# Optimization experiments

Measured on AMD Instinct MI355X. Metric: run time of the kernel, lower is better.

## Reference

```python
import jax, jax.numpy as jnp
import numpy as np

B, N_OBJ, K, D_MSG = 1024, 128, 32, 64
Y0 = 0.28209479177387814  # 1/(2*sqrt(pi)), l=0 integral-normalized SH
Y1 = 0.4886025119029199   # sqrt(3/(4*pi)),  l=1 integral-normalized SH


def _sh_lmax1(vec):
    """Spherical harmonics up to l=1, normalize=True, 'integral' normalization. [...,3] -> [...,4]."""
    r = jnp.linalg.norm(vec, axis=-1, keepdims=True)
    u = vec / jnp.maximum(r, 1e-12)
    return jnp.concatenate([jnp.full_like(r, Y0), Y1 * u], axis=-1)


def _forward(inputs, W_msg, W_out):
    Bsz, n, _ = inputs.shape
    masses = inputs[..., 0:1]           # [B,n,1]
    loc = inputs[..., 1:4]              # [B,n,3]
    vel = inputs[..., 4:7]              # [B,n,3]
    # canonicalize_mode == 'com': weights = masses
    w = masses
    com = jnp.sum(w / jnp.sum(w, axis=-2, keepdims=True) * loc, axis=-2, keepdims=True)
    loc = loc - com
    # --- knn_graph per batch element (loop=False, k nearest excluding self) ---
    d2 = jnp.sum((loc[:, :, None, :] - loc[:, None, :, :]) ** 2, axis=-1)  # [B,n,n]
    d2 = jnp.where(jnp.eye(n, dtype=bool)[None], jnp.inf, d2)
    _, nbr = jax.lax.top_k(-d2, K)                                          # [B,n,K]
    offs = (jnp.arange(Bsz) * n)[:, None, None]
    src = (nbr + offs).reshape(-1)                                          # edge_index[0]: neighbor j
    dst = (jnp.broadcast_to(jnp.arange(n)[None, :, None], (Bsz, n, K)) + offs).reshape(-1)  # edge_index[1]: center i
    # --- flatten node tensors ---
    pos = loc.reshape(-1, 3)
    v = vel.reshape(-1, 3)
    m = masses.reshape(-1, 1)
    Nn = Bsz * n
    # --- gravity graph augmentation ---
    rel = pos[src] - pos[dst]
    edge_dist = jnp.linalg.norm(rel, axis=-1, keepdims=True)
    prod_mass = m[src] * m[dst]
    edge_attr = _sh_lmax1(rel)                                              # [E,4]
    vel_emb = _sh_lmax1(v)                                                  # [Nn,4]
    deg = jnp.maximum(jax.ops.segment_sum(jnp.ones(src.shape[0], jnp.float32), dst, num_segments=Nn), 1.0)[:, None]
    node_attr = jax.ops.segment_sum(edge_attr, dst, num_segments=Nn) / deg + vel_emb
    vel_abs = jnp.linalg.norm(v, axis=-1, keepdims=True)
    x = jnp.concatenate([pos, v, vel_abs], axis=-1)                         # [Nn,7]
    amf = jnp.concatenate([edge_dist, prod_mass], axis=-1)                  # [E,2]
    # --- surrogate SEGNN: one message-passing layer ---
    m_in = jnp.concatenate([x[src], x[dst], edge_attr, amf], axis=-1)       # [E,20]
    msg = jax.nn.relu(m_in @ W_msg)                                         # [E,64]
    agg = jax.ops.segment_sum(msg, dst, num_segments=Nn) / deg              # [Nn,64]
    pred_shift = jnp.concatenate([x, node_attr, agg], axis=-1) @ W_out      # [Nn,3]
    return loc + pred_shift.reshape(Bsz, n, 3) + com


def setup_inputs() -> dict:
    key = jax.random.key(0)
    k1, k2, k3 = jax.random.split(key, 3)
    inputs = jax.random.uniform(k1, (B, N_OBJ, 7), dtype=jnp.float32)  # positive masses in col 0
    W_msg = jax.random.normal(k2, (20, D_MSG), dtype=jnp.float32) * 0.1
    W_out = jax.random.normal(k3, (D_MSG + 7 + 4, 3), dtype=jnp.float32) * 0.1
    return {"inputs": inputs, "W_msg": W_msg, "W_out": W_out}


def reference(inputs, W_msg, W_out):
    pred = _forward(inputs, W_msg, W_out)
    return (pred, jnp.zeros(inputs.shape[0], dtype=jnp.float32))
```

## Files before the change

kernel.cpp:

```cpp
#include <hip/hip_runtime.h>

#define NB 1024
#define NN 128
#define KK 32
#define DM 64

constexpr float Y0 = 0.28209479177387814f;
constexpr float Y1 = 0.4886025119029199f;

typedef float f2 __attribute__((ext_vector_type(2)));


__global__ __launch_bounds__(256) void k12_prep_knn(const float* __restrict__ in,
        float* __restrict__ feats, float* __restrict__ com, int* __restrict__ nbr,
        float* __restrict__ out)
{
    const int b = blockIdx.x, t = threadIdx.x;
    const int lane = t & 63, w = t >> 6;
    __shared__ float4 sP[128];
    __shared__ float red[2][4];

    float m=0.f,lx=0.f,ly=0.f,lz=0.f,vx=0.f,vy=0.f,vz=0.f;
    if (t < 128) {
        const float* p = in + ((size_t)b*NN + t)*7;
        m=p[0]; lx=p[1]; ly=p[2]; lz=p[3]; vx=p[4]; vy=p[5]; vz=p[6];
    }
    {
        float sw=m, sx=m*lx, sy=m*ly, sz=m*lz;
        #pragma unroll
        for (int s=1;s<64;s<<=1) {
            sw+=__shfl_xor(sw,s); sx+=__shfl_xor(sx,s);
            sy+=__shfl_xor(sy,s); sz+=__shfl_xor(sz,s);
        }
        if (t<128 && lane==0) { red[w][0]=sw; red[w][1]=sx; red[w][2]=sy; red[w][3]=sz; }
    }
    if (t==0) out[(size_t)NB*NN*3 + b] = 0.f;
    __syncthreads();
    const float Wt  = red[0][0]+red[1][0];
    const float cmx = (red[0][1]+red[1][1])/Wt;
    const float cmy = (red[0][2]+red[1][2])/Wt;
    const float cmz = (red[0][3]+red[1][3])/Wt;
    if (t < 128) {
        const float px=lx-cmx, py=ly-cmy, pz=lz-cmz;
        const float va = sqrtf(vx*vx+vy*vy+vz*vz);
        sP[t] = make_float4(px,py,pz,m);
        float4* f4 = (float4*)(feats + ((size_t)b*NN + t)*8);
        f4[0] = make_float4(px,py,pz,vx);
        f4[1] = make_float4(vy,vz,va,m);
        if (t==0) { float4* c4=(float4*)(com + (size_t)b*4); *c4 = make_float4(cmx,cmy,cmz,0.f); }
    }
    __syncthreads();

    const float4 A4 = sP[lane];
    const float4 B4 = sP[lane+64];
    const float INF = __int_as_float(0x7f800000);
    const unsigned long long lt = (1ULL<<lane)-1ULL;
    #pragma unroll 1
    for (int i=0; i<32; i+=4) {
        const int nb0 = w*32 + i;
        unsigned ua[4], ub[4], P[4];
        #pragma unroll
        for (int k=0;k<4;k++) {
            const int n = nb0 + k;
            const float4 C = sP[n];
            float dx=A4.x-C.x, dy=A4.y-C.y, dz=A4.z-C.z;
            float d2a = dx*dx+dy*dy+dz*dz;
            dx=B4.x-C.x; dy=B4.y-C.y; dz=B4.z-C.z;
            float d2b = dx*dx+dy*dy+dz*dz;
            if (lane    == n) d2a = INF;
            if (lane+64 == n) d2b = INF;
            ua[k]=__float_as_uint(d2a); ub[k]=__float_as_uint(d2b);
            P[k]=0u;
        }
        #pragma unroll 1
        for (int bit=30;bit>=0;--bit) {
            const unsigned msk = 1u<<bit;
            #pragma unroll
            for (int k=0;k<4;k++) {
                const unsigned Q = P[k]|msk;
                const int cnt = __popcll(__ballot(ua[k]<Q)) + __popcll(__ballot(ub[k]<Q));
                if (cnt<=31) P[k]=Q;
            }
        }
        #pragma unroll
        for (int k=0;k<4;k++) {
            const unsigned T = P[k];
            const unsigned long long m0=__ballot(ua[k]<T), m1=__ballot(ub[k]<T);
            const unsigned long long e0=__ballot(ua[k]==T), e1=__ballot(ub[k]==T);
            const int c0n=__popcll(m0), c=c0n+__popcll(m1), rem=32-c;
            int* row = nbr + ((size_t)b*NN + nb0 + k)*32;
            if (ua[k]< T) row[__popcll(m0&lt)] = lane;
            if (ub[k]< T) row[c0n+__popcll(m1&lt)] = lane+64;
            if (ua[k]==T) { const int r=__popcll(e0&lt);               if (r<rem) row[c+r]=lane; }
            if (ub[k]==T) { const int r=__popcll(e0)+__popcll(e1&lt);  if (r<rem) row[c+r]=lane+64; }
        }
    }
}

__global__ __launch_bounds__(256) void k3_main(const float* __restrict__ feats,
        const int* __restrict__ nbr, const float* __restrict__ Wm,
        const float* __restrict__ Wo, const float* __restrict__ com,
        float* __restrict__ out)
{
    const int b = blockIdx.x, t = threadIdx.x;
    __shared__ float4 sPos[128];
    __shared__ float4 sVel[128];
    __shared__ __align__(16) float sXs[128*64];
    __shared__ float  sWm[20][64];
    __shared__ float  sWo[75][3];
    __shared__ float4 sE4[32][33];
    __shared__ float  sPm[32][33];
    __shared__ int    sSrc[32][33];
    __shared__ float4 sSu[32];

    for (int i=t;i<1280;i+=256) ((float*)sWm)[i] = Wm[i];
    for (int i=t;i<225; i+=256) ((float*)sWo)[i] = Wo[i];
    if (t < 128) {
        const float4* f4 = (const float4*)(feats + ((size_t)b*NN + t)*8);
        sPos[t] = f4[0];
        sVel[t] = f4[1];
    }
    __syncthreads();
    if (t < 128) {
        const float4 a = sPos[t], c = sVel[t];
        sPos[t] = make_float4(a.x,a.y,a.z,c.w);
        sVel[t] = make_float4(a.w,c.x,c.y,c.z);
    }
    __syncthreads();

    for (int i=t;i<8192;i+=256) {
        const int n = i>>6, d = i&63;
        const float4 P = sPos[n], V = sVel[n];
        float s = P.x*sWm[0][d];
        s = fmaf(P.y, sWm[1][d], s);
        s = fmaf(P.z, sWm[2][d], s);
        s = fmaf(V.x, sWm[3][d], s);
        s = fmaf(V.y, sWm[4][d], s);
        s = fmaf(V.z, sWm[5][d], s);
        s = fmaf(V.w, sWm[6][d], s);
        const int q = d>>2;
        sXs[(n<<6) + ((q ^ (n&7))<<2) + (d&3)] = s;
    }
    __syncthreads();

    const int dsub = t & 7, ng = t >> 3, d0 = dsub*8, q0 = dsub*2;
    f2 wc2[5][4];
    #pragma unroll
    for (int r=0;r<5;r++)
        #pragma unroll
        for (int j=0;j<4;j++) {
            wc2[r][j].x = sWm[15+r][d0+2*j];
            wc2[r][j].y = sWm[15+r][d0+2*j+1];
        }
    const float cmx = com[(size_t)b*4+0], cmy = com[(size_t)b*4+1], cmz = com[(size_t)b*4+2];

    #pragma unroll 1
    for (int ch=0; ch<4; ++ch) {
        {
            const int nl = t>>3, j0 = (t&7)*4;
            const int n  = ch*32 + nl;
            const float4 Pn = sPos[n];
            const int4 nb4 = *(const int4*)(nbr + ((size_t)b*NN + n)*32 + j0);
            const int js[4] = {nb4.x, nb4.y, nb4.z, nb4.w};
            float sx=0.f, sy=0.f, sz=0.f;
            #pragma unroll
            for (int r=0;r<4;r++) {
                const int s = js[r];
                const float4 Ps = sPos[s];
                const float rx=Ps.x-Pn.x, ry=Ps.y-Pn.y, rz=Ps.z-Pn.z;
                const float dist = sqrtf(rx*rx+ry*ry+rz*rz);
                const float inv  = Y1 * __builtin_amdgcn_rcpf(fmaxf(dist,1e-12f));
                const float ux=rx*inv, uy=ry*inv, uz=rz*inv;
                sx+=ux; sy+=uy; sz+=uz;
                sE4[nl][j0+r] = make_float4(ux,uy,uz,dist);
                sPm[nl][j0+r] = Ps.w*Pn.w;
                sSrc[nl][j0+r] = s;
            }
            #pragma unroll
            for (int s=1;s<8;s<<=1) { sx+=__shfl_xor(sx,s); sy+=__shfl_xor(sy,s); sz+=__shfl_xor(sz,s); }
            if ((t&7)==0) sSu[nl] = make_float4(sx,sy,sz,0.f);
        }
        __syncthreads();

        {
            const int n = ch*32 + ng;
            const float4 Pn = sPos[n], Vn = sVel[n];
            f2 xdb2[4];
            #pragma unroll
            for (int j=0;j<4;j++) {
                #pragma unroll
                for (int h=0;h<2;h++) {
                    const int c = 2*j+h;
                    float s = Y0 * sWm[14][d0+c];
                    s = fmaf(Pn.x, sWm[7][d0+c], s);
                    s = fmaf(Pn.y, sWm[8][d0+c], s);
                    s = fmaf(Pn.z, sWm[9][d0+c], s);
                    s = fmaf(Vn.x, sWm[10][d0+c], s);
                    s = fmaf(Vn.y, sWm[11][d0+c], s);
                    s = fmaf(Vn.z, sWm[12][d0+c], s);
                    s = fmaf(Vn.w, sWm[13][d0+c], s);
                    if (h==0) xdb2[j].x = s; else xdb2[j].y = s;
                }
            }
            f2 acc2[4];
            #pragma unroll
            for (int j=0;j<4;j++) acc2[j] = (f2){0.f,0.f};
            const f2 zero2 = (f2){0.f,0.f};
            #pragma unroll 8
            for (int e=0;e<32;e++) {
                const float4 E = sE4[ng][e];
                const float pm = sPm[ng][e];
                const int s = sSrc[ng][e];
                const int a0 = (s<<8) + ((q0 ^ (s&7))<<4);
                const float4 xsA = *(const float4*)((const char*)sXs + a0);
                const float4 xsB = *(const float4*)((const char*)sXs + (a0^16));
                f2 xs2[4];
                xs2[0] = (f2){xsA.x, xsA.y};
                xs2[1] = (f2){xsA.z, xsA.w};
                xs2[2] = (f2){xsB.x, xsB.y};
                xs2[3] = (f2){xsB.z, xsB.w};
                const f2 ex = (f2){E.x, E.x};
                const f2 ey = (f2){E.y, E.y};
                const f2 ez = (f2){E.z, E.z};
                const f2 ew = (f2){E.w, E.w};
                const f2 pm2 = (f2){pm, pm};
                #pragma unroll
                for (int j=0;j<4;j++) {
                    f2 v = xdb2[j] + xs2[j];
                    v = __builtin_elementwise_fma(ex,  wc2[0][j], v);
                    v = __builtin_elementwise_fma(ey,  wc2[1][j], v);
                    v = __builtin_elementwise_fma(ez,  wc2[2][j], v);
                    v = __builtin_elementwise_fma(ew,  wc2[3][j], v);
                    v = __builtin_elementwise_fma(pm2, wc2[4][j], v);
                    v = __builtin_elementwise_max(v, zero2);
                    acc2[j] += v;
                }
            }
            float p0=0.f,p1=0.f,p2=0.f;
            #pragma unroll
            for (int j=0;j<4;j++) {
                const float a0v = acc2[j].x*(1.0f/32.0f);
                const float a1v = acc2[j].y*(1.0f/32.0f);
                const int c0 = 2*j, c1 = 2*j+1;
                p0 = fmaf(a0v, sWo[11+d0+c0][0], p0);
                p1 = fmaf(a0v, sWo[11+d0+c0][1], p1);
                p2 = fmaf(a0v, sWo[11+d0+c0][2], p2);
                p0 = fmaf(a1v, sWo[11+d0+c1][0], p0);
                p1 = fmaf(a1v, sWo[11+d0+c1][1], p1);
                p2 = fmaf(a1v, sWo[11+d0+c1][2], p2);
            }
            #pragma unroll
            for (int s=1;s<8;s<<=1) {
                p0 += __shfl_xor(p0,s); p1 += __shfl_xor(p1,s); p2 += __shfl_xor(p2,s);
            }
            if (dsub == 0) {
                const float4 Su = sSu[ng];
                const float vinv = Y1 * __builtin_amdgcn_rcpf(fmaxf(Vn.w,1e-12f));
                const float na0 = 2.f*Y0;
                const float na1 = Su.x*(1.f/32.f) + Vn.x*vinv;
                const float na2 = Su.y*(1.f/32.f) + Vn.y*vinv;
                const float na3 = Su.z*(1.f/32.f) + Vn.z*vinv;
                const float xf[7] = {Pn.x,Pn.y,Pn.z,Vn.x,Vn.y,Vn.z,Vn.w};
                #pragma unroll
                for (int k=0;k<7;k++) {
                    p0 = fmaf(xf[k], sWo[k][0], p0);
                    p1 = fmaf(xf[k], sWo[k][1], p1);
                    p2 = fmaf(xf[k], sWo[k][2], p2);
                }
                p0 += na0*sWo[7][0] + na1*sWo[8][0] + na2*sWo[9][0] + na3*sWo[10][0];
                p1 += na0*sWo[7][1] + na1*sWo[8][1] + na2*sWo[9][1] + na3*sWo[10][1];
                p2 += na0*sWo[7][2] + na1*sWo[8][2] + na2*sWo[9][2] + na3*sWo[10][2];
                float* op = out + ((size_t)b*NN + n)*3;
                op[0] = Pn.x + cmx + p0;
                op[1] = Pn.y + cmy + p1;
                op[2] = Pn.z + cmz + p2;
            }
        }
        __syncthreads();
    }
}

extern "C" void kernel_launch(void* const* d_in, const int* in_sizes, int n_in,
                              void* d_out, int out_size, void* d_ws, size_t ws_size,
                              hipStream_t stream)
{
    const float* in = (const float*)d_in[0];
    const float* Wm = (const float*)d_in[1];
    const float* Wo = (const float*)d_in[2];
    float* out = (float*)d_out;
    float* feats = (float*)d_ws;
    float* com   = feats + (size_t)NB*NN*8;
    int*   nbr   = (int*)(com + (size_t)NB*4);

    k12_prep_knn<<<NB, 256, 0, stream>>>(in, feats, com, nbr, out);
    k3_main     <<<NB, 256, 0, stream>>>(feats, nbr, Wm, Wo, com, out);
}
```

Before: 198.8 us.

## Replace radix-select kNN with bitonic sort in separate kernel, byte indices

Splits the prep and kNN stages into separate kernels and launches the kNN over four blocks per batch element. The bitwise radix select is replaced by a wavefront bitonic sort of 64-bit (distance, index) keys across 128 candidates. Neighbor indices are stored as bytes to shrink the index buffer and the reads in the main kernel. The cost is an extra launch and a global round trip for the features, and the sort performs many 64-bit shuffles per query row.

```diff
diff --git a/kernel.cpp b/kernel.cpp
--- a/kernel.cpp
+++ b/kernel.cpp
@@ -9,96 +9,104 @@
 constexpr float Y1 = 0.4886025119029199f;
 
 typedef float f2 __attribute__((ext_vector_type(2)));
-
-
-__global__ __launch_bounds__(256) void k12_prep_knn(const float* __restrict__ in,
-        float* __restrict__ feats, float* __restrict__ com, int* __restrict__ nbr,
-        float* __restrict__ out)
+typedef unsigned long long ull;
+
+
+__global__ __launch_bounds__(128) void k1_prep(const float* __restrict__ in,
+        float* __restrict__ feats, float* __restrict__ com, float* __restrict__ out)
 {
     const int b = blockIdx.x, t = threadIdx.x;
+    const float* p = in + ((size_t)b*NN + t)*7;
+    const float m  = p[0];
+    const float lx = p[1], ly = p[2], lz = p[3];
+    const float vx = p[4], vy = p[5], vz = p[6];
+    float w=m, wx=m*lx, wy=m*ly, wz=m*lz;
+    #pragma unroll
+    for (int s=1; s<64; s<<=1) {
+        w  += __shfl_xor(w,  s);
+        wx += __shfl_xor(wx, s);
+        wy += __shfl_xor(wy, s);
+        wz += __shfl_xor(wz, s);
+    }
+    __shared__ float red[2][4];
+    if ((t & 63) == 0) { int wi=t>>6; red[wi][0]=w; red[wi][1]=wx; red[wi][2]=wy; red[wi][3]=wz; }
+    __syncthreads();
+    const float Wt = red[0][0]+red[1][0];
+    const float cx = (red[0][1]+red[1][1])/Wt;
+    const float cy = (red[0][2]+red[1][2])/Wt;
+    const float cz = (red[0][3]+red[1][3])/Wt;
+    const float px = lx-cx, py = ly-cy, pz = lz-cz;
+    const float va = sqrtf(vx*vx+vy*vy+vz*vz);
+    float4* f4 = (float4*)(feats + ((size_t)b*NN + t)*8);
+    f4[0] = make_float4(px,py,pz,vx);
+    f4[1] = make_float4(vy,vz,va,m);
+    if (t==0) { float4* c4=(float4*)(com + (size_t)b*4); *c4 = make_float4(cx,cy,cz,0.f); }
+    if (b < 8) out[(size_t)NB*NN*3 + (size_t)b*128 + t] = 0.f;
+}
+
+__device__ __forceinline__ ull sx64(ull v, int m) {
+    return ((ull)(unsigned)__shfl_xor((int)(v>>32), m) << 32)
+         |       (unsigned)__shfl_xor((int)(v & 0xffffffffu), m);
+}
+
+__device__ __forceinline__ void ce(ull& k, int lane, int stride, bool asc) {
+    const ull p = sx64(k, stride);
+    const bool lower   = (lane & stride) == 0;
+    const bool keepmin = (lower == asc);
+    const bool less    = (k < p);
+    const bool take_p  = keepmin ? !less : less;
+    k = take_p ? p : k;
+}
+
+__global__ __launch_bounds__(256) void k2_knn(const float* __restrict__ feats,
+                                              unsigned char* __restrict__ nbr)
+{
+    const int b = blockIdx.x >> 2, qtr = blockIdx.x & 3;
+    const int t = threadIdx.x;
     const int lane = t & 63, w = t >> 6;
     __shared__ float4 sP[128];
-    __shared__ float red[2][4];
-
-    float m=0.f,lx=0.f,ly=0.f,lz=0.f,vx=0.f,vy=0.f,vz=0.f;
-    if (t < 128) {
-        const float* p = in + ((size_t)b*NN + t)*7;
-        m=p[0]; lx=p[1]; ly=p[2]; lz=p[3]; vx=p[4]; vy=p[5]; vz=p[6];
-    }
-    {
-        float sw=m, sx=m*lx, sy=m*ly, sz=m*lz;
+    if (t < 128) sP[t] = *(const float4*)(feats + ((size_t)b*NN + t)*8);
+    __syncthreads();
+    const float4 A = sP[lane];
+    const float4 B = sP[lane+64];
+    const float INF = __int_as_float(0x7f800000);
+
+    #pragma unroll 1
+    for (int i=0; i<8; ++i) {
+        const int n = qtr*32 + w*8 + i;
+        const float4 C = sP[n];
+        float dx=A.x-C.x, dy=A.y-C.y, dz=A.z-C.z;
+        float d2a = dx*dx+dy*dy+dz*dz;
+        dx=B.x-C.x; dy=B.y-C.y; dz=B.z-C.z;
+        float d2b = dx*dx+dy*dy+dz*dz;
+        if (lane    == n) d2a = INF;
+        if (lane+64 == n) d2b = INF;
+        ull k0 = ((ull)__float_as_uint(d2a) << 32) | (unsigned)lane;
+        ull k1 = ((ull)__float_as_uint(d2b) << 32) | (unsigned)(lane+64);
+
         #pragma unroll
-        for (int s=1;s<64;s<<=1) {
-            sw+=__shfl_xor(sw,s); sx+=__shfl_xor(sx,s);
-            sy+=__shfl_xor(sy,s); sz+=__shfl_xor(sz,s);
-        }
-        if (t<128 && lane==0) { red[w][0]=sw; red[w][1]=sx; red[w][2]=sy; red[w][3]=sz; }
-    }
-    if (t==0) out[(size_t)NB*NN*3 + b] = 0.f;
-    __syncthreads();
-    const float Wt  = red[0][0]+red[1][0];
-    const float cmx = (red[0][1]+red[1][1])/Wt;
-    const float cmy = (red[0][2]+red[1][2])/Wt;
-    const float cmz = (red[0][3]+red[1][3])/Wt;
-    if (t < 128) {
-        const float px=lx-cmx, py=ly-cmy, pz=lz-cmz;
-        const float va = sqrtf(vx*vx+vy*vy+vz*vz);
-        sP[t] = make_float4(px,py,pz,m);
-        float4* f4 = (float4*)(feats + ((size_t)b*NN + t)*8);
-        f4[0] = make_float4(px,py,pz,vx);
-        f4[1] = make_float4(vy,vz,va,m);
-        if (t==0) { float4* c4=(float4*)(com + (size_t)b*4); *c4 = make_float4(cmx,cmy,cmz,0.f); }
-    }
-    __syncthreads();
-
-    const float4 A4 = sP[lane];
-    const float4 B4 = sP[lane+64];
-    const float INF = __int_as_float(0x7f800000);
-    const unsigned long long lt = (1ULL<<lane)-1ULL;
-    #pragma unroll 1
-    for (int i=0; i<32; i+=4) {
-        const int nb0 = w*32 + i;
-        unsigned ua[4], ub[4], P[4];
+        for (int size = 2; size <= 64; size <<= 1) {
+            #pragma unroll
+            for (int stride = size >> 1; stride >= 1; stride >>= 1) {
+                const bool asc0 = (lane & size) == 0;
+                const bool asc1 = (size == 64) ? false : asc0;
+                ce(k0, lane, stride, asc0);
+                ce(k1, lane, stride, asc1);
+            }
+        }
+        if (k0 > k1) { const ull tmp = k0; k0 = k1; k1 = tmp; }
         #pragma unroll
-        for (int k=0;k<4;k++) {
-            const int n = nb0 + k;
-            const float4 C = sP[n];
-            float dx=A4.x-C.x, dy=A4.y-C.y, dz=A4.z-C.z;
-            float d2a = dx*dx+dy*dy+dz*dz;
-            dx=B4.x-C.x; dy=B4.y-C.y; dz=B4.z-C.z;
-            float d2b = dx*dx+dy*dy+dz*dz;
-            if (lane    == n) d2a = INF;
-            if (lane+64 == n) d2b = INF;
-            ua[k]=__float_as_uint(d2a); ub[k]=__float_as_uint(d2b);
-            P[k]=0u;
-        }
-        #pragma unroll 1
-        for (int bit=30;bit>=0;--bit) {
-            const unsigned msk = 1u<<bit;
-            #pragma unroll
-            for (int k=0;k<4;k++) {
-                const unsigned Q = P[k]|msk;
-                const int cnt = __popcll(__ballot(ua[k]<Q)) + __popcll(__ballot(ub[k]<Q));
-                if (cnt<=31) P[k]=Q;
-            }
-        }
-        #pragma unroll
-        for (int k=0;k<4;k++) {
-            const unsigned T = P[k];
-            const unsigned long long m0=__ballot(ua[k]<T), m1=__ballot(ub[k]<T);
-            const unsigned long long e0=__ballot(ua[k]==T), e1=__ballot(ub[k]==T);
-            const int c0n=__popcll(m0), c=c0n+__popcll(m1), rem=32-c;
-            int* row = nbr + ((size_t)b*NN + nb0 + k)*32;
-            if (ua[k]< T) row[__popcll(m0&lt)] = lane;
-            if (ub[k]< T) row[c0n+__popcll(m1&lt)] = lane+64;
-            if (ua[k]==T) { const int r=__popcll(e0&lt);               if (r<rem) row[c+r]=lane; }
-            if (ub[k]==T) { const int r=__popcll(e0)+__popcll(e1&lt);  if (r<rem) row[c+r]=lane+64; }
-        }
+        for (int stride = 32; stride >= 1; stride >>= 1) {
+            ce(k0, lane, stride, true);
+            ce(k1, lane, stride, true);
+        }
+        if (lane < 32)
+            nbr[((size_t)b*NN + n)*32 + lane] = (unsigned char)(k0 & 0xffu);
     }
 }
 
 __global__ __launch_bounds__(256) void k3_main(const float* __restrict__ feats,
-        const int* __restrict__ nbr, const float* __restrict__ Wm,
+        const unsigned char* __restrict__ nbr, const float* __restrict__ Wm,
         const float* __restrict__ Wo, const float* __restrict__ com,
         float* __restrict__ out)
 {
@@ -160,7 +168,7 @@
             const int nl = t>>3, j0 = (t&7)*4;
             const int n  = ch*32 + nl;
             const float4 Pn = sPos[n];
-            const int4 nb4 = *(const int4*)(nbr + ((size_t)b*NN + n)*32 + j0);
+            const uchar4 nb4 = *(const uchar4*)(nbr + ((size_t)b*NN + n)*32 + j0);
             const int js[4] = {nb4.x, nb4.y, nb4.z, nb4.w};
             float sx=0.f, sy=0.f, sz=0.f;
             #pragma unroll
@@ -290,8 +298,9 @@
     float* out = (float*)d_out;
     float* feats = (float*)d_ws;
     float* com   = feats + (size_t)NB*NN*8;
-    int*   nbr   = (int*)(com + (size_t)NB*4);
-
-    k12_prep_knn<<<NB, 256, 0, stream>>>(in, feats, com, nbr, out);
-    k3_main     <<<NB, 256, 0, stream>>>(feats, nbr, Wm, Wo, com, out);
-}
+    unsigned char* nbr = (unsigned char*)(com + (size_t)NB*4);
+
+    k1_prep<<<NB,   128, 0, stream>>>(in, feats, com, out);
+    k2_knn <<<NB*4, 256, 0, stream>>>(feats, nbr);
+    k3_main<<<NB,   256, 0, stream>>>(feats, nbr, Wm, Wo, com, out);
+}
```

New measurement: 266.0 us. 33.8% more time.
